# Kernel optimization log

Hardware: AMD Instinct MI355X
Metric: run time of the kernel (lower is better)

## Reference

```python
import jax, jax.numpy as jnp
import numpy as np

B, S, HS, HHS, NH = 128, 8000, 9, 8, 4
HD = HHS // NH  # head dim = 2


def _layernorm(x, g, b, eps=1e-6):
    m = jnp.mean(x, axis=-1, keepdims=True)
    v = jnp.mean((x - m) ** 2, axis=-1, keepdims=True)
    return (x - m) * jax.lax.rsqrt(v + eps) * g + b


def _binding(a, b):
    # HRR binding: circular convolution along last dim
    return jnp.fft.ifft(jnp.fft.fft(a) * jnp.fft.fft(b)).real


def _unbinding(s, a):
    # HRR unbinding: circular correlation along last dim
    return jnp.fft.ifft(jnp.fft.fft(s) * jnp.conj(jnp.fft.fft(a))).real


def _cosine_sim(a, b, eps=1e-8):
    num = jnp.sum(a * b, axis=-1, keepdims=True)
    na = jnp.maximum(jnp.linalg.norm(a, axis=-1, keepdims=True), eps)
    nb = jnp.maximum(jnp.linalg.norm(b, axis=-1, keepdims=True), eps)
    return num / (na * nb)


def _heads(x):  # [B,S,HHS] -> [B,NH,S,HD]
    return x.reshape(B, S, NH, HD).transpose(0, 2, 1, 3)


def setup_inputs() -> dict:
    key = jax.random.key(0)
    ks = jax.random.split(key, 12)
    p = {}
    p["x"] = jax.random.normal(ks[0], (B, S, HS), dtype=jnp.float32)
    p["mask"] = jnp.ones((B, NH, S, 1), dtype=jnp.float32)
    p["pos_bias"] = jax.random.normal(ks[1], (1, S, HS), dtype=jnp.float32) * 0.02
    p["ln_g"] = jnp.ones((HS,), dtype=jnp.float32)
    p["ln_b"] = jnp.zeros((HS,), dtype=jnp.float32)
    p["Wq"] = jax.random.normal(ks[2], (HHS, HS), dtype=jnp.float32) * 0.3
    p["bq"] = jnp.zeros((HHS,), dtype=jnp.float32)
    p["Wk"] = jax.random.normal(ks[3], (HHS, HS), dtype=jnp.float32) * 0.3
    p["bk"] = jnp.zeros((HHS,), dtype=jnp.float32)
    p["Wv"] = jax.random.normal(ks[4], (HHS, HS), dtype=jnp.float32) * 0.3
    p["bv"] = jnp.zeros((HHS,), dtype=jnp.float32)
    p["W1"] = jax.random.normal(ks[5], (HS, HHS), dtype=jnp.float32) * 0.3
    p["b1"] = jnp.zeros((HS,), dtype=jnp.float32)
    p["W2"] = jax.random.normal(ks[6], (HS, HHS), dtype=jnp.float32) * 0.3
    p["b2"] = jnp.zeros((HS,), dtype=jnp.float32)
    p["Wo"] = jax.random.normal(ks[7], (1, HS), dtype=jnp.float32) * 0.3
    p["bo"] = jnp.zeros((1,), dtype=jnp.float32)
    return p


def reference(x, mask, pos_bias, ln_g, ln_b, Wq, bq, Wk, bk, Wv, bv, W1, b1, W2, b2, Wo, bo):
    x = x + pos_bias
    x = _layernorm(x, ln_g, ln_b)
    q = _heads(x @ Wq.T + bq)  # [B,NH,S,HD]
    k = _heads(x @ Wk.T + bk)
    v = _heads(x @ Wv.T + bv)
    bind = _binding(k, v).sum(axis=-2, keepdims=True)  # [B,NH,1,HD]
    vp = _unbinding(bind, q)                            # [B,NH,S,HD]
    scale = _cosine_sim(v, vp)                          # [B,NH,S,1]
    scale = scale + (1.0 - mask) * -1e9
    weight = jax.nn.softmax(scale, axis=-2)             # softmax over S
    weighted = weight * v                               # [B,NH,S,HD]
    attn_out = weighted.transpose(0, 2, 1, 3).reshape(B, S, HHS)
    # NOTE: original has dead code h=ffn1(attn_out); h=layernorm(h+x)
    # which is immediately overwritten and does not affect the output.
    h = jax.nn.gelu(attn_out @ W2.T + b2, approximate=False) + x
    return h @ Wo.T + bo  # [B,S,1]
```

## Files before the change

kernel.cpp:

```cpp
#include <hip/hip_runtime.h>
#include <math.h>

#define TB 256
#define S_LEN 8000
#define B_N 128
#define BPB 8
#define TPB 4
#define GRID (B_N * BPB)
#define CTRW 32


__device__ __forceinline__ void matvec89(const float* __restrict__ W, const float* __restrict__ bias,
                                         const float* __restrict__ y, float* out) {
#pragma unroll
  for (int i = 0; i < 8; ++i) {
    float a = bias[i];
#pragma unroll
    for (int j = 0; j < 9; ++j) a += W[i * 9 + j] * y[j];
    out[i] = a;
  }
}

__device__ __forceinline__ float head_scale(const float* q, const float* v, const float* bindS,
                                            int h, float maskv) {
  float q0 = q[2 * h], q1 = q[2 * h + 1];
  float v0 = v[2 * h], v1 = v[2 * h + 1];
  float B0 = bindS[2 * h], B1 = bindS[2 * h + 1];
  float vp0 = B0 * q0 + B1 * q1;
  float vp1 = B0 * q1 + B1 * q0;
  float num = v0 * vp0 + v1 * vp1;
  float a2 = fmaxf(v0 * v0 + v1 * v1, 1e-16f);
  float b2 = fmaxf(vp0 * vp0 + vp1 * vp1, 1e-16f);
  float sc = num * rsqrtf(a2 * b2);
  sc += (1.f - maskv) * (-1e9f);
  return sc;
}

__device__ __forceinline__ void batch_barrier(unsigned* ctr, int tid) {
  __syncthreads();
  if (tid == 0) {
    __hip_atomic_fetch_add(ctr, 1u, __ATOMIC_RELAXED, __HIP_MEMORY_SCOPE_AGENT);
    while (__hip_atomic_load(ctr, __ATOMIC_RELAXED, __HIP_MEMORY_SCOPE_AGENT) < (unsigned)BPB)
      __builtin_amdgcn_s_sleep(1);
  }
  __syncthreads();
}
__device__ __forceinline__ void barrier_arrive(unsigned* ctr, int tid) {
  __syncthreads();
  if (tid == 0)
    __hip_atomic_fetch_add(ctr, 1u, __ATOMIC_RELAXED, __HIP_MEMORY_SCOPE_AGENT);
}
__device__ __forceinline__ void barrier_wait(unsigned* ctr, int tid) {
  if (tid == 0) {
    while (__hip_atomic_load(ctr, __ATOMIC_RELAXED, __HIP_MEMORY_SCOPE_AGENT) < (unsigned)BPB)
      __builtin_amdgcn_s_sleep(1);
  }
  __syncthreads();
}

__global__ void k_init(unsigned* __restrict__ ctrs, float* __restrict__ gws,
                       const float* __restrict__ W2, const float* __restrict__ b2,
                       const float* __restrict__ Wo, const float* __restrict__ bo) {
  int tid = blockIdx.x * blockDim.x + threadIdx.x;
  if (tid < 2 * B_N * CTRW) ctrs[tid] = 0u;
  if (blockIdx.x == 0 && threadIdx.x == 0) {
    float G[8];
#pragma unroll
    for (int j = 0; j < 8; ++j) G[j] = 0.f;
    float C0 = bo[0];
#pragma unroll
    for (int i = 0; i < 9; ++i) {
      float b = b2[i];
      float Phi = 0.5f * (1.f + erff(b * 0.70710678118654752f));
      float phi = 0.39894228040143268f * __expf(-0.5f * b * b);
      C0 += Wo[i] * (b * Phi);
      float wg = Wo[i] * (Phi + b * phi);
#pragma unroll
      for (int j = 0; j < 8; ++j) G[j] += wg * W2[i * 8 + j];
    }
#pragma unroll
    for (int j = 0; j < 8; ++j) gws[j] = G[j];
    gws[8] = C0;
  }
}

__global__ __launch_bounds__(TB, 4) void k_fused(
    const float* __restrict__ x, const float* __restrict__ mask, const float* __restrict__ pos,
    const float* __restrict__ lng, const float* __restrict__ lnb,
    const float* __restrict__ Wq, const float* __restrict__ bq,
    const float* __restrict__ Wk, const float* __restrict__ bk,
    const float* __restrict__ Wv, const float* __restrict__ bv,
    const float* __restrict__ Wo,
    const float* __restrict__ gws,
    unsigned* __restrict__ ctr1, unsigned* __restrict__ ctr2,
    float* __restrict__ bindP, float* __restrict__ sumP,
    float* __restrict__ out) {
  __shared__ float red[4 * 8];
  __shared__ float sib[BPB * 8];
  __shared__ float bindS[8], invDS[4];

  const int tid = threadIdx.x, bid = blockIdx.x;
  const int b = bid >> 3;
  const int t0 = (bid & 7) * TPB;
  const int wave = tid >> 6, lane = tid & 63;
  const float* maskb = mask + (size_t)b * 4 * S_LEN;

  int nrowA[TPB];
#pragma unroll
  for (int t = 0; t < TPB; ++t) nrowA[t] = min(TB, S_LEN - (t0 + t) * TB);

  float y[TPB][9];
  float vv[TPB][8];
  float acc[8];
#pragma unroll
  for (int i = 0; i < 8; ++i) acc[i] = 0.f;

#pragma unroll
  for (int t = 0; t < TPB; ++t) {
    if (tid < nrowA[t]) {
      const int s = (t0 + t) * TB + tid;
      const float* xr = x + ((size_t)b * S_LEN + s) * 9;
      const float* pr = pos + (size_t)s * 9;
      float m = 0.f;
#pragma unroll
      for (int j = 0; j < 9; ++j) { y[t][j] = xr[j] + pr[j]; m += y[t][j]; }
      m *= (1.f / 9.f);
      float var = 0.f;
#pragma unroll
      for (int j = 0; j < 9; ++j) { float d = y[t][j] - m; var += d * d; }
      var *= (1.f / 9.f);
      float rs = rsqrtf(var + 1e-6f);
#pragma unroll
      for (int j = 0; j < 9; ++j) y[t][j] = (y[t][j] - m) * rs * lng[j] + lnb[j];

      float kk[8];
      matvec89(Wk, bk, y[t], kk);
      matvec89(Wv, bv, y[t], vv[t]);
#pragma unroll
      for (int h = 0; h < 4; ++h) {
        float k0 = kk[2 * h], k1 = kk[2 * h + 1];
        float v0 = vv[t][2 * h], v1 = vv[t][2 * h + 1];
        acc[2 * h]     += k0 * v0 + k1 * v1;
        acc[2 * h + 1] += k0 * v1 + k1 * v0;
      }
    }
  }
#pragma unroll
  for (int i = 0; i < 8; ++i) {
#pragma unroll
    for (int off = 32; off > 0; off >>= 1) acc[i] += __shfl_down(acc[i], off, 64);
  }
  __syncthreads();
  if (lane == 0) {
#pragma unroll
    for (int i = 0; i < 8; ++i) red[wave * 8 + i] = acc[i];
  }
  __syncthreads();
  if (tid < 8) {
    float s = red[tid] + red[8 + tid] + red[16 + tid] + red[24 + tid];
    __hip_atomic_store(&bindP[bid * 8 + tid], s, __ATOMIC_RELAXED, __HIP_MEMORY_SCOPE_AGENT);
  }

  barrier_arrive(&ctr1[b * CTRW], tid);

  float mm[TPB][4];
#pragma unroll
  for (int t = 0; t < TPB; ++t) {
    const int s = (t0 + t) * TB + tid;
    if (tid < nrowA[t]) {
#pragma unroll
      for (int h = 0; h < 4; ++h) mm[t][h] = maskb[(size_t)h * S_LEN + s];
    }
  }
  float qq[TPB][8];
  float gv[TPB][4];
  float oy[TPB];
#pragma unroll
  for (int t = 0; t < TPB; ++t) {
#pragma unroll
    for (int h = 0; h < 4; ++h) gv[t][h] = 0.f;
    oy[t] = 0.f;
    if (tid < nrowA[t]) {
      matvec89(Wq, bq, y[t], qq[t]);
      float o = 0.f;
#pragma unroll
      for (int i = 0; i < 9; ++i) o += Wo[i] * y[t][i];
      oy[t] = o;
#pragma unroll
      for (int h = 0; h < 4; ++h)
        gv[t][h] = gws[2 * h] * vv[t][2 * h] + gws[2 * h + 1] * vv[t][2 * h + 1];
    }
  }

  barrier_wait(&ctr1[b * CTRW], tid);

  if (tid < BPB * 8)
    sib[tid] = __hip_atomic_load(&bindP[(size_t)b * BPB * 8 + tid],
                                 __ATOMIC_RELAXED, __HIP_MEMORY_SCOPE_AGENT);
  __syncthreads();
  if (tid < 8) {
    float s = 0.f;
#pragma unroll
    for (int j = 0; j < BPB; ++j) s += sib[j * 8 + tid];
    bindS[tid] = s;
  }
  __syncthreads();

  float e[TPB][4];
  float esum[4] = {0.f, 0.f, 0.f, 0.f};
#pragma unroll
  for (int t = 0; t < TPB; ++t) {
#pragma unroll
    for (int h = 0; h < 4; ++h) e[t][h] = 0.f;
    if (tid < nrowA[t]) {
#pragma unroll
      for (int h = 0; h < 4; ++h) {
        e[t][h] = __expf(head_scale(qq[t], vv[t], bindS, h, mm[t][h]));
        esum[h] += e[t][h];
      }
    }
  }
#pragma unroll
  for (int h = 0; h < 4; ++h) {
#pragma unroll
    for (int off = 32; off > 0; off >>= 1) esum[h] += __shfl_down(esum[h], off, 64);
  }
  __syncthreads();
  if (lane == 0) {
#pragma unroll
    for (int h = 0; h < 4; ++h) red[wave * 4 + h] = esum[h];
  }
  __syncthreads();
  if (tid < 4) {
    float s = red[tid] + red[4 + tid] + red[8 + tid] + red[12 + tid];
    __hip_atomic_store(&sumP[bid * 4 + tid], s, __ATOMIC_RELAXED, __HIP_MEMORY_SCOPE_AGENT);
  }

  batch_barrier(&ctr2[b * CTRW], tid);

  if (tid < BPB * 4)
    sib[tid] = __hip_atomic_load(&sumP[(size_t)b * BPB * 4 + tid],
                                 __ATOMIC_RELAXED, __HIP_MEMORY_SCOPE_AGENT);
  __syncthreads();
  if (tid < 4) {
    float s = 0.f;
#pragma unroll
    for (int j = 0; j < BPB; ++j) s += sib[j * 4 + tid];
    invDS[tid] = 1.f / s;
  }
  __syncthreads();

  const float C0 = gws[8];
#pragma unroll
  for (int t = 0; t < TPB; ++t) {
    const int s0 = (t0 + t) * TB;
    if (tid < nrowA[t]) {
      float o = C0 + oy[t];
#pragma unroll
      for (int h = 0; h < 4; ++h) o += (e[t][h] * invDS[h]) * gv[t][h];
      out[(size_t)b * S_LEN + s0 + tid] = o;
    }
  }
}


extern "C" void kernel_launch(void* const* d_in, const int* in_sizes, int n_in,
                              void* d_out, int out_size, void* d_ws, size_t ws_size,
                              hipStream_t stream) {
  const float* x    = (const float*)d_in[0];
  const float* mask = (const float*)d_in[1];
  const float* pos  = (const float*)d_in[2];
  const float* lng  = (const float*)d_in[3];
  const float* lnb  = (const float*)d_in[4];
  const float* Wq   = (const float*)d_in[5];
  const float* bq   = (const float*)d_in[6];
  const float* Wk   = (const float*)d_in[7];
  const float* bk   = (const float*)d_in[8];
  const float* Wv   = (const float*)d_in[9];
  const float* bv   = (const float*)d_in[10];
  const float* W2   = (const float*)d_in[13];
  const float* b2   = (const float*)d_in[14];
  const float* Wo   = (const float*)d_in[15];
  const float* bo   = (const float*)d_in[16];
  float* out = (float*)d_out;

  unsigned* ctr1  = (unsigned*)d_ws;
  unsigned* ctr2  = ctr1 + B_N * CTRW;
  float*    gws   = (float*)(ctr2 + B_N * CTRW);
  float*    bindP = gws + 16;
  float*    sumP  = bindP + GRID * 8;

  k_init<<<(2 * B_N * CTRW + 255) / 256, 256, 0, stream>>>(ctr1, gws, W2, b2, Wo, bo);
  k_fused<<<GRID, TB, 0, stream>>>(x, mask, pos, lng, lnb, Wq, bq, Wk, bk, Wv, bv,
                                   Wo, gws, ctr1, ctr2, bindP, sumP, out);
}
```

Measured before the change: 30.72 us.

## Fold init kernel into fused kernel, split second barrier, use transpose-style wave reductions

```diff
diff --git a/kernel.cpp b/kernel.cpp
--- a/kernel.cpp
+++ b/kernel.cpp
@@ -36,15 +36,53 @@
   return sc;
 }
 
-__device__ __forceinline__ void batch_barrier(unsigned* ctr, int tid) {
-  __syncthreads();
-  if (tid == 0) {
-    __hip_atomic_fetch_add(ctr, 1u, __ATOMIC_RELAXED, __HIP_MEMORY_SCOPE_AGENT);
-    while (__hip_atomic_load(ctr, __ATOMIC_RELAXED, __HIP_MEMORY_SCOPE_AGENT) < (unsigned)BPB)
-      __builtin_amdgcn_s_sleep(1);
-  }
-  __syncthreads();
-}
+__device__ __forceinline__ float wave_reduce8(const float* acc, int lane) {
+  float s4[4];
+#pragma unroll
+  for (int i = 0; i < 4; ++i) {
+    bool hi = lane & 1;
+    float send = hi ? acc[2 * i] : acc[2 * i + 1];
+    float keep = hi ? acc[2 * i + 1] : acc[2 * i];
+    s4[i] = keep + __shfl_xor(send, 1, 64);
+  }
+  float s2[2];
+#pragma unroll
+  for (int j = 0; j < 2; ++j) {
+    bool hi = lane & 2;
+    float send = hi ? s4[2 * j] : s4[2 * j + 1];
+    float keep = hi ? s4[2 * j + 1] : s4[2 * j];
+    s2[j] = keep + __shfl_xor(send, 2, 64);
+  }
+  bool hi = lane & 4;
+  float send = hi ? s2[0] : s2[1];
+  float keep = hi ? s2[1] : s2[0];
+  float s1 = keep + __shfl_xor(send, 4, 64);
+  s1 += __shfl_xor(s1, 8, 64);
+  s1 += __shfl_xor(s1, 16, 64);
+  s1 += __shfl_xor(s1, 32, 64);
+  return s1;
+}
+
+__device__ __forceinline__ float wave_reduce4(const float* acc, int lane) {
+  float s2[2];
+#pragma unroll
+  for (int j = 0; j < 2; ++j) {
+    bool hi = lane & 1;
+    float send = hi ? acc[2 * j] : acc[2 * j + 1];
+    float keep = hi ? acc[2 * j + 1] : acc[2 * j];
+    s2[j] = keep + __shfl_xor(send, 1, 64);
+  }
+  bool hi = lane & 2;
+  float send = hi ? s2[0] : s2[1];
+  float keep = hi ? s2[1] : s2[0];
+  float s1 = keep + __shfl_xor(send, 2, 64);
+  s1 += __shfl_xor(s1, 4, 64);
+  s1 += __shfl_xor(s1, 8, 64);
+  s1 += __shfl_xor(s1, 16, 64);
+  s1 += __shfl_xor(s1, 32, 64);
+  return s1;
+}
+
 __device__ __forceinline__ void barrier_arrive(unsigned* ctr, int tid) {
   __syncthreads();
   if (tid == 0)
@@ -56,32 +94,6 @@
       __builtin_amdgcn_s_sleep(1);
   }
   __syncthreads();
-}
-
-__global__ void k_init(unsigned* __restrict__ ctrs, float* __restrict__ gws,
-                       const float* __restrict__ W2, const float* __restrict__ b2,
-                       const float* __restrict__ Wo, const float* __restrict__ bo) {
-  int tid = blockIdx.x * blockDim.x + threadIdx.x;
-  if (tid < 2 * B_N * CTRW) ctrs[tid] = 0u;
-  if (blockIdx.x == 0 && threadIdx.x == 0) {
-    float G[8];
-#pragma unroll
-    for (int j = 0; j < 8; ++j) G[j] = 0.f;
-    float C0 = bo[0];
-#pragma unroll
-    for (int i = 0; i < 9; ++i) {
-      float b = b2[i];
-      float Phi = 0.5f * (1.f + erff(b * 0.70710678118654752f));
-      float phi = 0.39894228040143268f * __expf(-0.5f * b * b);
-      C0 += Wo[i] * (b * Phi);
-      float wg = Wo[i] * (Phi + b * phi);
-#pragma unroll
-      for (int j = 0; j < 8; ++j) G[j] += wg * W2[i * 8 + j];
-    }
-#pragma unroll
-    for (int j = 0; j < 8; ++j) gws[j] = G[j];
-    gws[8] = C0;
-  }
 }
 
 __global__ __launch_bounds__(TB, 4) void k_fused(
@@ -90,20 +102,41 @@
     const float* __restrict__ Wq, const float* __restrict__ bq,
     const float* __restrict__ Wk, const float* __restrict__ bk,
     const float* __restrict__ Wv, const float* __restrict__ bv,
-    const float* __restrict__ Wo,
-    const float* __restrict__ gws,
+    const float* __restrict__ W2, const float* __restrict__ b2,
+    const float* __restrict__ Wo, const float* __restrict__ bo,
     unsigned* __restrict__ ctr1, unsigned* __restrict__ ctr2,
     float* __restrict__ bindP, float* __restrict__ sumP,
     float* __restrict__ out) {
   __shared__ float red[4 * 8];
   __shared__ float sib[BPB * 8];
   __shared__ float bindS[8], invDS[4];
+  __shared__ float gS[12];
 
   const int tid = threadIdx.x, bid = blockIdx.x;
   const int b = bid >> 3;
   const int t0 = (bid & 7) * TPB;
   const int wave = tid >> 6, lane = tid & 63;
   const float* maskb = mask + (size_t)b * 4 * S_LEN;
+
+  if (tid == 0) {
+    float G[8];
+#pragma unroll
+    for (int j = 0; j < 8; ++j) G[j] = 0.f;
+    float C0 = bo[0];
+#pragma unroll
+    for (int i = 0; i < 9; ++i) {
+      float bb = b2[i];
+      float Phi = 0.5f * (1.f + erff(bb * 0.70710678118654752f));
+      float phi = 0.39894228040143268f * __expf(-0.5f * bb * bb);
+      C0 += Wo[i] * (bb * Phi);
+      float wg = Wo[i] * (Phi + bb * phi);
+#pragma unroll
+      for (int j = 0; j < 8; ++j) G[j] += wg * W2[i * 8 + j];
+    }
+#pragma unroll
+    for (int j = 0; j < 8; ++j) gS[j] = G[j];
+    gS[8] = C0;
+  }
 
   int nrowA[TPB];
 #pragma unroll
@@ -145,15 +178,10 @@
       }
     }
   }
-#pragma unroll
-  for (int i = 0; i < 8; ++i) {
-#pragma unroll
-    for (int off = 32; off > 0; off >>= 1) acc[i] += __shfl_down(acc[i], off, 64);
-  }
-  __syncthreads();
-  if (lane == 0) {
-#pragma unroll
-    for (int i = 0; i < 8; ++i) red[wave * 8 + i] = acc[i];
+  {
+    float s1 = wave_reduce8(acc, lane);
+    __syncthreads();
+    if (lane < 8) red[wave * 8 + lane] = s1;
   }
   __syncthreads();
   if (tid < 8) {
@@ -188,7 +216,7 @@
       oy[t] = o;
 #pragma unroll
       for (int h = 0; h < 4; ++h)
-        gv[t][h] = gws[2 * h] * vv[t][2 * h] + gws[2 * h + 1] * vv[t][2 * h + 1];
+        gv[t][h] = gS[2 * h] * vv[t][2 * h] + gS[2 * h + 1] * vv[t][2 * h + 1];
     }
   }
 
@@ -220,15 +248,10 @@
       }
     }
   }
-#pragma unroll
-  for (int h = 0; h < 4; ++h) {
-#pragma unroll
-    for (int off = 32; off > 0; off >>= 1) esum[h] += __shfl_down(esum[h], off, 64);
-  }
-  __syncthreads();
-  if (lane == 0) {
-#pragma unroll
-    for (int h = 0; h < 4; ++h) red[wave * 4 + h] = esum[h];
+  {
+    float s1 = wave_reduce4(esum, lane);
+    __syncthreads();
+    if (lane < 4) red[wave * 4 + lane] = s1;
   }
   __syncthreads();
   if (tid < 4) {
@@ -236,7 +259,16 @@
     __hip_atomic_store(&sumP[bid * 4 + tid], s, __ATOMIC_RELAXED, __HIP_MEMORY_SCOPE_AGENT);
   }
 
-  batch_barrier(&ctr2[b * CTRW], tid);
+  barrier_arrive(&ctr2[b * CTRW], tid);
+
+  float egv[TPB][4];
+#pragma unroll
+  for (int t = 0; t < TPB; ++t) {
+#pragma unroll
+    for (int h = 0; h < 4; ++h) egv[t][h] = e[t][h] * gv[t][h];
+  }
+
+  barrier_wait(&ctr2[b * CTRW], tid);
 
   if (tid < BPB * 4)
     sib[tid] = __hip_atomic_load(&sumP[(size_t)b * BPB * 4 + tid],
@@ -250,14 +282,14 @@
   }
   __syncthreads();
 
-  const float C0 = gws[8];
+  const float C0 = gS[8];
 #pragma unroll
   for (int t = 0; t < TPB; ++t) {
     const int s0 = (t0 + t) * TB;
     if (tid < nrowA[t]) {
       float o = C0 + oy[t];
 #pragma unroll
-      for (int h = 0; h < 4; ++h) o += (e[t][h] * invDS[h]) * gv[t][h];
+      for (int h = 0; h < 4; ++h) o += egv[t][h] * invDS[h];
       out[(size_t)b * S_LEN + s0 + tid] = o;
     }
   }
@@ -286,11 +318,10 @@
 
   unsigned* ctr1  = (unsigned*)d_ws;
   unsigned* ctr2  = ctr1 + B_N * CTRW;
-  float*    gws   = (float*)(ctr2 + B_N * CTRW);
-  float*    bindP = gws + 16;
+  float*    bindP = (float*)(ctr2 + B_N * CTRW);
   float*    sumP  = bindP + GRID * 8;
 
-  k_init<<<(2 * B_N * CTRW + 255) / 256, 256, 0, stream>>>(ctr1, gws, W2, b2, Wo, bo);
+  hipMemsetAsync(d_ws, 0, 2 * B_N * CTRW * sizeof(unsigned), stream);
   k_fused<<<GRID, TB, 0, stream>>>(x, mask, pos, lng, lnb, Wq, bq, Wk, bk, Wv, bv,
-                                   Wo, gws, ctr1, ctr2, bindP, sumP, out);
-}
+                                   W2, b2, Wo, bo, ctr1, ctr2, bindP, sumP, out);
+}
```

After: 31.03 us. About the same (+1.0%).
